# Kernel tuning notes

Hardware: AMD Instinct MI355X
Metric: run time of the kernel (lower is better)

The kernel has to match this reference:

```python
import jax, jax.numpy as jnp
import numpy as np

B, T, C = 2, 2048, 2048
E, K, S, F = 8, 2, 1, 1408
AUX_COEF, Z_COEF = 0.01, 0.001


def setup_inputs() -> dict:
    key = jax.random.key(0)
    ks = jax.random.split(key, 8)
    sc = 1.0 / np.sqrt(C)
    sf = 1.0 / np.sqrt(F)
    return {
        "x": jax.random.normal(ks[0], (B, T, C), jnp.float32),
        "gate_w": jax.random.normal(ks[1], (E, C), jnp.float32) * sc,   # torch Linear weight [out,in]
        "w1": jax.random.normal(ks[2], (E, F, C), jnp.float32) * sc,    # routed expert up-proj
        "w2": jax.random.normal(ks[3], (E, C, F), jnp.float32) * sf,    # routed expert down-proj
        "sw1": jax.random.normal(ks[4], (S, F, C), jnp.float32) * sc,   # shared expert up-proj
        "sw2": jax.random.normal(ks[5], (S, C, F), jnp.float32) * sf,   # shared expert down-proj
        "alpha": jnp.ones((C,), jnp.float32),                            # HyperConnection scale on MoE out
        "beta": jnp.ones((C,), jnp.float32),                             # HyperConnection scale on residual x
    }


def reference(x, gate_w, w1, w2, sw1, sw2, alpha, beta):
    Bv, Tv, Cv = x.shape
    xf = x.reshape(-1, Cv)                                  # [N, C]
    logits = xf @ gate_w.T                                  # [N, E]
    probs = jax.nn.softmax(logits, axis=-1)
    weights, selected = jax.lax.top_k(probs, K)             # [N, K]
    weights = weights / jnp.sum(weights, axis=-1, keepdims=True)
    aux_loss = AUX_COEF * jnp.sum(jnp.mean(probs, axis=0) ** 2)
    z_loss = Z_COEF * jnp.mean(jax.nn.logsumexp(logits, axis=-1) ** 2)
    # combine[n, e] = routing weight of expert e for token n (0 if not selected)
    combine = jnp.sum(jax.nn.one_hot(selected, E, dtype=xf.dtype) * weights[..., None], axis=1)  # [N, E]
    out = jnp.zeros_like(xf)
    for e in range(E):  # fixed small expert count; weight is 0 for unrouted tokens
        h = jax.nn.silu(xf @ w1[e].T) @ w2[e].T             # [N, C]
        out = out + combine[:, e:e + 1] * h
    for s in range(S):
        out = out + jax.nn.silu(xf @ sw1[s].T) @ sw2[s].T
    y = alpha * out.reshape(Bv, Tv, Cv) + beta * x           # HyperConnection residual mix
    return y, aux_loss + z_loss
```

## Files before the change

kernel.cpp:

```cpp
#include <hip/hip_runtime.h>


#define TOKS 4096
#define CD 2048
#define FD 1408
#define RROWS 8192
#define NTMAX 104

typedef unsigned short u16;
typedef float f32x4 __attribute__((ext_vector_type(4)));
typedef __bf16 bf16x8 __attribute__((ext_vector_type(8)));

__device__ __forceinline__ u16 f2bf(float f) {
  unsigned u = __float_as_uint(f);
  u += 0x7fffu + ((u >> 16) & 1u);
  return (u16)(u >> 16);
}

__global__ __launch_bounds__(256) void gate_kernel(
    const float* __restrict__ x, const float* __restrict__ gw,
    float* __restrict__ combine, float* __restrict__ part, int* __restrict__ sel,
    u16* __restrict__ xb)
{
  const int lane = threadIdx.x & 63;
  const int wave = threadIdx.x >> 6;
  const int n = blockIdx.x * 4 + wave;
  const float* xr = x + (size_t)n * CD;
  u16* xbr = xb + (size_t)n * CD;
  float p[8] = {0,0,0,0,0,0,0,0};
#pragma unroll
  for (int it = 0; it < 8; ++it) {
    const int idx = it * 256 + lane * 4;
    const float4 xv = *(const float4*)(xr + idx);
    ushort4 xo;
    xo.x = f2bf(xv.x); xo.y = f2bf(xv.y); xo.z = f2bf(xv.z); xo.w = f2bf(xv.w);
    *(ushort4*)(xbr + idx) = xo;
#pragma unroll
    for (int e = 0; e < 8; ++e) {
      const float4 gv = *(const float4*)(gw + e * CD + idx);
      p[e] += xv.x * gv.x + xv.y * gv.y + xv.z * gv.z + xv.w * gv.w;
    }
  }
#pragma unroll
  for (int e = 0; e < 8; ++e) {
#pragma unroll
    for (int m = 32; m > 0; m >>= 1) p[e] += __shfl_xor(p[e], m, 64);
  }
  float mx = p[0];
#pragma unroll
  for (int e = 1; e < 8; ++e) mx = fmaxf(mx, p[e]);
  float s = 0.f, pr[8];
#pragma unroll
  for (int e = 0; e < 8; ++e) { pr[e] = __expf(p[e] - mx); s += pr[e]; }
  const float inv = 1.f / s;
#pragma unroll
  for (int e = 0; e < 8; ++e) pr[e] *= inv;
  const float lse = mx + __logf(s);
  int i1 = 0;
#pragma unroll
  for (int e = 1; e < 8; ++e) if (pr[e] > pr[i1]) i1 = e;
  int i2 = (i1 == 0) ? 1 : 0;
#pragma unroll
  for (int e = 0; e < 8; ++e) if (e != i1 && pr[e] > pr[i2]) i2 = e;
  const float rs = 1.f / (pr[i1] + pr[i2]);

  __shared__ float pl[4][12];
  if (lane == 0) {
    float* cr = combine + (size_t)n * 16;
#pragma unroll
    for (int e = 0; e < 8; ++e) cr[e] = 0.f;
    cr[i1] = pr[i1] * rs;
    cr[i2] = pr[i2] * rs;
    cr[8] = 1.0f;
    sel[n] = i1 | (i2 << 4);
#pragma unroll
    for (int e = 0; e < 8; ++e) pl[wave][e] = pr[e];
    pl[wave][8] = lse * lse;
  }
  __syncthreads();
  if (threadIdx.x < 9)
    part[(size_t)blockIdx.x * 16 + threadIdx.x] =
        pl[0][threadIdx.x] + pl[1][threadIdx.x] + pl[2][threadIdx.x] + pl[3][threadIdx.x];
}

__global__ void route_kernel(const int* __restrict__ sel, int* __restrict__ le,
                             int* __restrict__ pos, int* __restrict__ cntoff,
                             int* __restrict__ tileMap)
{
  const int lane = threadIdx.x;
  const unsigned long long lt = (1ull << lane) - 1ull;
  int cnt[8] = {0,0,0,0,0,0,0,0};
  for (int c = 0; c < TOKS / 64; ++c) {
    const int s = sel[c * 64 + lane];
    const int e1 = s & 15, e2 = (s >> 4) & 15;
#pragma unroll
    for (int e = 0; e < 8; ++e)
      cnt[e] += __popcll(__ballot(e1 == e)) + __popcll(__ballot(e2 == e));
  }
  int off[8]; off[0] = 0;
#pragma unroll
  for (int e = 1; e < 8; ++e) off[e] = off[e - 1] + cnt[e - 1];
  int base[8];
#pragma unroll
  for (int e = 0; e < 8; ++e) base[e] = off[e];
  for (int c = 0; c < TOKS / 64; ++c) {
    const int n = c * 64 + lane;
    const int s = sel[n];
    const int e1 = s & 15, e2 = (s >> 4) & 15;
#pragma unroll
    for (int e = 0; e < 8; ++e) {
      const unsigned long long m1 = __ballot(e1 == e);
      const unsigned long long m2 = __ballot(e2 == e);
      if (e1 == e) { const int r = base[e] + __popcll(m1 & lt); le[r] = n; pos[2 * n] = r; }
      if (e2 == e) { const int r = base[e] + __popcll(m1) + __popcll(m2 & lt); le[r] = n; pos[2 * n + 1] = r; }
      base[e] += __popcll(m1) + __popcll(m2);
    }
  }
  if (lane < 8) { cntoff[lane] = cnt[lane]; cntoff[16 + lane] = off[lane]; }
  if (lane == 8) { cntoff[8] = TOKS; cntoff[24] = RROWS; }
  if (lane == 0) {
    int t = 0;
    for (int e = 0; e < 8; ++e)
      for (int m = 0; m < cnt[e]; m += 128) tileMap[t++] = e | (m << 4);
    for (int m = 0; m < TOKS; m += 128) tileMap[t++] = 8 | (m << 4);
    cntoff[25] = t;
  }
}

__global__ void finalize_kernel(const float* __restrict__ part, float* __restrict__ loss_out)
{
  __shared__ float sm[256][10];
  float loc[9] = {0,0,0,0,0,0,0,0,0};
  for (int b = threadIdx.x; b < 1024; b += 256)
#pragma unroll
    for (int c = 0; c < 9; ++c) loc[c] += part[(size_t)b * 16 + c];
#pragma unroll
  for (int c = 0; c < 9; ++c) sm[threadIdx.x][c] = loc[c];
  __syncthreads();
  for (int off = 128; off > 0; off >>= 1) {
    if (threadIdx.x < off)
#pragma unroll
      for (int c = 0; c < 9; ++c) sm[threadIdx.x][c] += sm[threadIdx.x + off][c];
    __syncthreads();
  }
  if (threadIdx.x == 0) {
    float aux = 0.f;
#pragma unroll
    for (int e = 0; e < 8; ++e) { const float m = sm[0][e] * (1.f / TOKS); aux += m * m; }
    const float z = sm[0][8] * (1.f / TOKS);
    loss_out[0] = 0.01f * aux + 0.001f * z;
  }
}

#define W14  5767168
#define SW14 720896
__global__ void cast_all_kernel(const float4* __restrict__ w1, const float4* __restrict__ sw1,
                                const float4* __restrict__ w2, const float4* __restrict__ sw2,
                                u16* __restrict__ w1b, u16* __restrict__ w2b)
{
  const int total = 2 * (W14 + SW14);
  int i = blockIdx.x * blockDim.x + threadIdx.x;
  const int stride = gridDim.x * blockDim.x;
  for (; i < total; i += stride) {
    int j = i;
    const float4* src; u16* dst;
    if (j < W14)                   { src = w1;  dst = w1b; }
    else if ((j -= W14) < SW14)    { src = sw1; dst = w1b + (size_t)8 * FD * CD; }
    else if ((j -= SW14) < W14)    { src = w2;  dst = w2b; }
    else                           { j -= W14; src = sw2; dst = w2b + (size_t)8 * CD * FD; }
    const float4 v = src[j];
    ushort4 o;
    o.x = f2bf(v.x); o.y = f2bf(v.y); o.z = f2bf(v.z); o.w = f2bf(v.w);
    *(ushort4*)(dst + (size_t)j * 4) = o;
  }
}

template<int MODE, int MINW>
__global__ __launch_bounds__(256, MINW) void gemm_bt(
    const u16* __restrict__ Abase, const u16* __restrict__ Bbase,
    u16* __restrict__ outBF, const float* __restrict__ combine,
    const int* __restrict__ le, const int* __restrict__ cntoff,
    const int* __restrict__ tileMap)
{
  constexpr int K  = (MODE == 0) ? CD : FD;
  constexpr int OS = (MODE == 0) ? FD : CD;
  constexpr int NY = (MODE == 0) ? 11 : 16;
  constexpr int Q  = NTMAX * NY / 8;

  __shared__ __attribute__((aligned(16))) u16 smA[128 * 64];
  __shared__ __attribute__((aligned(16))) u16 smB[128 * 64];

  const int orig = blockIdx.x + gridDim.x * blockIdx.y;
  const int wgid = (orig & 7) * Q + (orig >> 3);
  const int t = wgid / NY;
  const int y = wgid - t * NY;
  const int NT = cntoff[25];
  if (t >= NT) return;
  const int packed = tileMap[t];
  const int e = packed & 15;
  const int m0 = packed >> 4;
  const int cnt = cntoff[e];
  const int off = cntoff[16 + e];
  const int n0 = y * 128;

  const int tid = threadIdx.x;
  const int lane = tid & 63;
  const int wave = tid >> 6;
  const int wr = wave >> 1, wc = wave & 1;

  const u16* A = (MODE == 0) ? Abase : (Abase + (size_t)off * FD);
  const u16* Bp = Bbase + (size_t)e * FD * CD;

  const int sub_r = lane >> 3;
  const int sub_c = (lane & 7) << 3;

  int arow[4];
#pragma unroll
  for (int r = 0; r < 4; ++r) {
    const int lr = (wave * 4 + r) * 8 + sub_r;
    if (MODE == 0)
      arow[r] = (e == 8) ? (m0 + lr) : ((m0 + lr < cnt) ? le[off + m0 + lr] : 0);
    else
      arow[r] = m0 + lr;
  }

  f32x4 acc[4][4] = {};

  const int nkt = K >> 6;
  for (int kt = 0; kt < nkt; ++kt) {
    const int k0 = kt << 6;
#pragma unroll
    for (int r = 0; r < 4; ++r) {
      const int ch = (wave << 2) + r;
      const u16* ga = A + (size_t)arow[r] * K + k0 + sub_c;
      const u16* gb = Bp + (size_t)(n0 + ch * 8 + sub_r) * K + k0 + sub_c;
      __builtin_amdgcn_global_load_lds((const __attribute__((address_space(1))) void*)ga,
                                       (__attribute__((address_space(3))) void*)(smA + ch * 512),
                                       16, 0, 0);
      __builtin_amdgcn_global_load_lds((const __attribute__((address_space(1))) void*)gb,
                                       (__attribute__((address_space(3))) void*)(smB + ch * 512),
                                       16, 0, 0);
    }
    asm volatile("s_waitcnt vmcnt(0)" ::: "memory");
    __syncthreads();
#pragma unroll
    for (int kk = 0; kk < 2; ++kk) {
      const int ko = (kk << 5) + ((lane >> 4) << 3);
      bf16x8 af[4];
#pragma unroll
      for (int i = 0; i < 4; ++i)
        af[i] = *(const bf16x8*)(smA + ((wr * 64 + i * 16 + (lane & 15)) << 6) + ko);
#pragma unroll
      for (int j = 0; j < 4; ++j) {
        const bf16x8 bv = *(const bf16x8*)(smB + ((wc * 64 + j * 16 + (lane & 15)) << 6) + ko);
#pragma unroll
        for (int i = 0; i < 4; ++i)
          acc[i][j] = __builtin_amdgcn_mfma_f32_16x16x32_bf16(af[i], bv, acc[i][j], 0, 0, 0);
      }
    }
    __syncthreads();
  }

#pragma unroll
  for (int i = 0; i < 4; ++i) {
    const int rloc0 = wr * 64 + i * 16 + ((lane >> 4) << 2);
#pragma unroll
    for (int q = 0; q < 4; ++q) {
      const int rloc = rloc0 + q;
      if (m0 + rloc >= cnt) continue;
      float sc = 1.f;
      if (MODE == 0) {
        const int tok = (e == 8) ? (m0 + rloc) : le[off + m0 + rloc];
        sc = combine[(size_t)tok * 16 + e];
      }
#pragma unroll
      for (int j = 0; j < 4; ++j) {
        const int col = n0 + wc * 64 + j * 16 + (lane & 15);
        const float v = acc[i][j][q];
        const float h = (MODE == 0) ? (sc * v * (1.f / (1.f + __expf(-v)))) : v;
        outBF[(size_t)(off + m0 + rloc) * OS + col] = f2bf(h);
      }
    }
  }
}

__global__ __launch_bounds__(256) void gather_kernel(
    const u16* __restrict__ Yc, const int* __restrict__ pos,
    const float* __restrict__ x, const float* __restrict__ alpha,
    const float* __restrict__ beta, float* __restrict__ out)
{
  const int n = blockIdx.x;
  const int c0 = threadIdx.x * 8;
  const int p1 = pos[2 * n], p2 = pos[2 * n + 1];
  const bf16x8 a = *(const bf16x8*)(Yc + (size_t)p1 * CD + c0);
  const bf16x8 b = *(const bf16x8*)(Yc + (size_t)p2 * CD + c0);
  const bf16x8 s = *(const bf16x8*)(Yc + ((size_t)RROWS + n) * CD + c0);
  const float* xr = x + (size_t)n * CD + c0;
  float* orow = out + (size_t)n * CD + c0;
#pragma unroll
  for (int j = 0; j < 8; ++j) {
    const float v = (float)a[j] + (float)b[j] + (float)s[j];
    orow[j] = alpha[c0 + j] * v + beta[c0 + j] * xr[j];
  }
}

extern "C" void kernel_launch(void* const* d_in, const int* in_sizes, int n_in,
                              void* d_out, int out_size, void* d_ws, size_t ws_size,
                              hipStream_t stream)
{
  (void)in_sizes; (void)n_in; (void)out_size; (void)ws_size;
  const float* x     = (const float*)d_in[0];
  const float* gw    = (const float*)d_in[1];
  const float* w1    = (const float*)d_in[2];
  const float* w2    = (const float*)d_in[3];
  const float* sw1   = (const float*)d_in[4];
  const float* sw2   = (const float*)d_in[5];
  const float* alpha = (const float*)d_in[6];
  const float* beta  = (const float*)d_in[7];
  float* out = (float*)d_out;

  char* ws = (char*)d_ws;
  float* combine = (float*)(ws + 0);
  float* part    = (float*)(ws + 262144);
  int*   sel     = (int*)(ws + 327680);
  int*   le      = (int*)(ws + 344064);
  int*   pos     = (int*)(ws + 376832);
  int*   cntoff  = (int*)(ws + 409600);
  int*   tileMap = (int*)(ws + 409856);
  u16*   xb      = (u16*)(ws + 410368);
  u16*   w1b     = (u16*)(ws + 17187584);
  u16*   w2b     = (u16*)(ws + 69092096);
  u16*   Hcomp   = (u16*)(ws + 120996608);
  u16*   Ycomp   = (u16*)(ws + 155599616);

  gate_kernel<<<1024, 256, 0, stream>>>(x, gw, combine, part, sel, xb);
  route_kernel<<<1, 64, 0, stream>>>(sel, le, pos, cntoff, tileMap);
  finalize_kernel<<<1, 256, 0, stream>>>(part, out + (size_t)TOKS * CD);
  cast_all_kernel<<<4096, 256, 0, stream>>>((const float4*)w1, (const float4*)sw1,
                                            (const float4*)w2, (const float4*)sw2, w1b, w2b);
  gemm_bt<0, 5><<<dim3(NTMAX, 11), 256, 0, stream>>>(xb, w1b, Hcomp, combine, le, cntoff, tileMap);
  gemm_bt<1, 4><<<dim3(NTMAX, 16), 256, 0, stream>>>(Hcomp, w2b, Ycomp, nullptr, nullptr, cntoff, tileMap);
  gather_kernel<<<TOKS, 256, 0, stream>>>(Ycomp, pos, x, alpha, beta, out);
}
```

Before: 498.3 us.

## Triple-buffer grouped GEMM with 256-row tiles, XOR-swizzled LDS and 512 threads

Reworks the grouped expert GEMM so each workgroup covers 256 token rows with 512 threads (8 waves). It uses a three-stage LDS ring filled by global_load_lds, with partial vmcnt waits so loads run two K-steps ahead of the MFMA work. LDS columns are XOR-swizzled to cut bank conflicts, and MFMA sections get raised priority. The aim is to hide global memory latency and halve B-operand traffic per row. The cost is more LDS use, fewer workgroups, more padding waste on small expert tiles, and out-of-range A rows that are clamped rather than skipped.

```diff
diff --git a/kernel.cpp b/kernel.cpp
--- a/kernel.cpp
+++ b/kernel.cpp
@@ -5,7 +5,7 @@
 #define CD 2048
 #define FD 1408
 #define RROWS 8192
-#define NTMAX 104
+#define NT256 56
 
 typedef unsigned short u16;
 typedef float f32x4 __attribute__((ext_vector_type(4)));
@@ -121,8 +121,8 @@
   if (lane == 0) {
     int t = 0;
     for (int e = 0; e < 8; ++e)
-      for (int m = 0; m < cnt[e]; m += 128) tileMap[t++] = e | (m << 4);
-    for (int m = 0; m < TOKS; m += 128) tileMap[t++] = 8 | (m << 4);
+      for (int m = 0; m < cnt[e]; m += 256) tileMap[t++] = e | (m << 4);
+    for (int m = 0; m < TOKS; m += 256) tileMap[t++] = 8 | (m << 4);
     cntoff[25] = t;
   }
 }
@@ -175,20 +175,21 @@
   }
 }
 
-template<int MODE, int MINW>
-__global__ __launch_bounds__(256, MINW) void gemm_bt(
+template<int MODE>
+__global__ __launch_bounds__(512, 2) void gemm_bt(
     const u16* __restrict__ Abase, const u16* __restrict__ Bbase,
     u16* __restrict__ outBF, const float* __restrict__ combine,
     const int* __restrict__ le, const int* __restrict__ cntoff,
     const int* __restrict__ tileMap)
 {
-  constexpr int K  = (MODE == 0) ? CD : FD;
-  constexpr int OS = (MODE == 0) ? FD : CD;
-  constexpr int NY = (MODE == 0) ? 11 : 16;
-  constexpr int Q  = NTMAX * NY / 8;
-
-  __shared__ __attribute__((aligned(16))) u16 smA[128 * 64];
-  __shared__ __attribute__((aligned(16))) u16 smB[128 * 64];
+  constexpr int K   = (MODE == 0) ? CD : FD;
+  constexpr int OS  = (MODE == 0) ? FD : CD;
+  constexpr int NY  = (MODE == 0) ? 11 : 16;
+  constexpr int NKT = K >> 6;
+  constexpr int Q   = NT256 * NY / 8;
+
+  __shared__ __attribute__((aligned(16))) u16 smA[3][256 * 64];
+  __shared__ __attribute__((aligned(16))) u16 smB[3][128 * 64];
 
   const int orig = blockIdx.x + gridDim.x * blockIdx.y;
   const int wgid = (orig & 7) * Q + (orig >> 3);
@@ -203,67 +204,106 @@
   const int off = cntoff[16 + e];
   const int n0 = y * 128;
 
-  const int tid = threadIdx.x;
+  const int tid  = threadIdx.x;
   const int lane = tid & 63;
   const int wave = tid >> 6;
-  const int wr = wave >> 1, wc = wave & 1;
-
-  const u16* A = (MODE == 0) ? Abase : (Abase + (size_t)off * FD);
+  const int wm = wave >> 1;
+  const int wn = wave & 1;
+
   const u16* Bp = Bbase + (size_t)e * FD * CD;
 
-  const int sub_r = lane >> 3;
-  const int sub_c = (lane & 7) << 3;
-
-  int arow[4];
-#pragma unroll
-  for (int r = 0; r < 4; ++r) {
-    const int lr = (wave * 4 + r) * 8 + sub_r;
+  const int srow = wave * 8 + (lane >> 3);
+  const int gcol = (((lane & 7) ^ ((lane >> 3) & 7)) << 3);
+
+  const u16* pAg[4];
+#pragma unroll
+  for (int c = 0; c < 4; ++c) {
+    const int r = m0 + c * 64 + srow;
+    long arow;
     if (MODE == 0)
-      arow[r] = (e == 8) ? (m0 + lr) : ((m0 + lr < cnt) ? le[off + m0 + lr] : 0);
+      arow = (e == 8) ? r : le[min(off + r, RROWS - 1)];
     else
-      arow[r] = m0 + lr;
-  }
+      arow = min(off + r, RROWS + TOKS - 1);
+    pAg[c] = Abase + (size_t)arow * K + gcol;
+  }
+  const u16* pBg[2];
+#pragma unroll
+  for (int c = 0; c < 2; ++c)
+    pBg[c] = Bp + (size_t)(n0 + c * 64 + srow) * K + gcol;
+
+  auto STG = [&](u16* pa, u16* pb, int kt) {
+    const int kof = kt << 6;
+#pragma unroll
+    for (int c = 0; c < 4; ++c)
+      __builtin_amdgcn_global_load_lds(
+          (const __attribute__((address_space(1))) void*)(pAg[c] + kof),
+          (__attribute__((address_space(3))) void*)(pa + c * 4096 + wave * 512), 16, 0, 0);
+#pragma unroll
+    for (int c = 0; c < 2; ++c)
+      __builtin_amdgcn_global_load_lds(
+          (const __attribute__((address_space(1))) void*)(pBg[c] + kof),
+          (__attribute__((address_space(3))) void*)(pb + c * 4096 + wave * 512), 16, 0, 0);
+  };
+
+  u16 *pa0 = smA[0], *pa1 = smA[1], *pa2 = smA[2];
+  u16 *pb0 = smB[0], *pb1 = smB[1], *pb2 = smB[2];
 
   f32x4 acc[4][4] = {};
 
-  const int nkt = K >> 6;
-  for (int kt = 0; kt < nkt; ++kt) {
-    const int k0 = kt << 6;
-#pragma unroll
-    for (int r = 0; r < 4; ++r) {
-      const int ch = (wave << 2) + r;
-      const u16* ga = A + (size_t)arow[r] * K + k0 + sub_c;
-      const u16* gb = Bp + (size_t)(n0 + ch * 8 + sub_r) * K + k0 + sub_c;
-      __builtin_amdgcn_global_load_lds((const __attribute__((address_space(1))) void*)ga,
-                                       (__attribute__((address_space(3))) void*)(smA + ch * 512),
-                                       16, 0, 0);
-      __builtin_amdgcn_global_load_lds((const __attribute__((address_space(1))) void*)gb,
-                                       (__attribute__((address_space(3))) void*)(smB + ch * 512),
-                                       16, 0, 0);
-    }
-    asm volatile("s_waitcnt vmcnt(0)" ::: "memory");
-    __syncthreads();
+  STG(pa0, pb0, 0);
+  STG(pa1, pb1, 1);
+
+  const int la15 = lane & 15;
+  const int g16  = lane >> 4;
+
+#pragma unroll 1
+  for (int kt = 0; kt < NKT; ++kt) {
+    if (kt + 2 < NKT) {
+      STG(pa2, pb2, kt + 2);
+      asm volatile("s_waitcnt vmcnt(12)" ::: "memory");
+    } else if (kt + 2 == NKT) {
+      asm volatile("s_waitcnt vmcnt(6)" ::: "memory");
+    } else {
+      asm volatile("s_waitcnt vmcnt(0)" ::: "memory");
+    }
+    asm volatile("" ::: "memory");
+    __builtin_amdgcn_s_barrier();
+    asm volatile("" ::: "memory");
+
 #pragma unroll
     for (int kk = 0; kk < 2; ++kk) {
-      const int ko = (kk << 5) + ((lane >> 4) << 3);
-      bf16x8 af[4];
+      const int gg = (kk << 2) + g16;
+      bf16x8 af[4], bv[4];
+#pragma unroll
+      for (int i = 0; i < 4; ++i) {
+        const int r = wm * 64 + i * 16 + la15;
+        af[i] = *(const bf16x8*)(pa0 + r * 64 + ((gg ^ (r & 7)) << 3));
+      }
+#pragma unroll
+      for (int j = 0; j < 4; ++j) {
+        const int r = wn * 64 + j * 16 + la15;
+        bv[j] = *(const bf16x8*)(pb0 + r * 64 + ((gg ^ (r & 7)) << 3));
+      }
+      __builtin_amdgcn_s_setprio(1);
 #pragma unroll
       for (int i = 0; i < 4; ++i)
-        af[i] = *(const bf16x8*)(smA + ((wr * 64 + i * 16 + (lane & 15)) << 6) + ko);
-#pragma unroll
-      for (int j = 0; j < 4; ++j) {
-        const bf16x8 bv = *(const bf16x8*)(smB + ((wc * 64 + j * 16 + (lane & 15)) << 6) + ko);
-#pragma unroll
-        for (int i = 0; i < 4; ++i)
-          acc[i][j] = __builtin_amdgcn_mfma_f32_16x16x32_bf16(af[i], bv, acc[i][j], 0, 0, 0);
-      }
-    }
-    __syncthreads();
+#pragma unroll
+        for (int j = 0; j < 4; ++j)
+          acc[i][j] = __builtin_amdgcn_mfma_f32_16x16x32_bf16(af[i], bv[j], acc[i][j], 0, 0, 0);
+      __builtin_amdgcn_s_setprio(0);
+    }
+
+    asm volatile("" ::: "memory");
+    __builtin_amdgcn_s_barrier();
+    asm volatile("" ::: "memory");
+
+    u16* ta = pa0; pa0 = pa1; pa1 = pa2; pa2 = ta;
+    u16* tb = pb0; pb0 = pb1; pb1 = pb2; pb2 = tb;
   }
 
 #pragma unroll
   for (int i = 0; i < 4; ++i) {
-    const int rloc0 = wr * 64 + i * 16 + ((lane >> 4) << 2);
+    const int rloc0 = wm * 64 + i * 16 + (g16 << 2);
 #pragma unroll
     for (int q = 0; q < 4; ++q) {
       const int rloc = rloc0 + q;
@@ -275,7 +315,7 @@
       }
 #pragma unroll
       for (int j = 0; j < 4; ++j) {
-        const int col = n0 + wc * 64 + j * 16 + (lane & 15);
+        const int col = n0 + wn * 64 + j * 16 + la15;
         const float v = acc[i][j][q];
         const float h = (MODE == 0) ? (sc * v * (1.f / (1.f + __expf(-v)))) : v;
         outBF[(size_t)(off + m0 + rloc) * OS + col] = f2bf(h);
@@ -338,7 +378,7 @@
   finalize_kernel<<<1, 256, 0, stream>>>(part, out + (size_t)TOKS * CD);
   cast_all_kernel<<<4096, 256, 0, stream>>>((const float4*)w1, (const float4*)sw1,
                                             (const float4*)w2, (const float4*)sw2, w1b, w2b);
-  gemm_bt<0, 5><<<dim3(NTMAX, 11), 256, 0, stream>>>(xb, w1b, Hcomp, combine, le, cntoff, tileMap);
-  gemm_bt<1, 4><<<dim3(NTMAX, 16), 256, 0, stream>>>(Hcomp, w2b, Ycomp, nullptr, nullptr, cntoff, tileMap);
+  gemm_bt<0><<<dim3(NT256, 11), 512, 0, stream>>>(xb, w1b, Hcomp, combine, le, cntoff, tileMap);
+  gemm_bt<1><<<dim3(NT256, 16), 512, 0, stream>>>(Hcomp, w2b, Ycomp, nullptr, nullptr, cntoff, tileMap);
   gather_kernel<<<TOKS, 256, 0, stream>>>(Ycomp, pos, x, alpha, beta, out);
 }
```

New measurement: 458.6 us. -8.0%, faster.

## Switch expert GEMMs to 256x256 tiles with double-buffered swizzled LDS and 8 waves

Applied to the files above, without the earlier changes.

Replaces the 128x128 single-buffered expert GEMM with a 512-thread kernel that computes 256x256 tiles. It double-buffers LDS with staged prefetch interleaved across four compute phases, XOR-swizzles the LDS layout to avoid bank conflicts, and raises MFMA priority with setprio. The up-projection weights are padded to 1536 rows so the N dimension divides into 256-wide tiles, with padded columns skipped at store time. The larger tiles improve data reuse and overlap loads with compute, but they add padding waste, partially empty M tiles for smaller experts, and fewer workgroups.

```diff
diff --git a/kernel.cpp b/kernel.cpp
--- a/kernel.cpp
+++ b/kernel.cpp
@@ -4,8 +4,9 @@
 #define TOKS 4096
 #define CD 2048
 #define FD 1408
+#define FDP 1536
 #define RROWS 8192
-#define NTMAX 104
+#define NT256 56
 
 typedef unsigned short u16;
 typedef float f32x4 __attribute__((ext_vector_type(4)));
@@ -121,8 +122,8 @@
   if (lane == 0) {
     int t = 0;
     for (int e = 0; e < 8; ++e)
-      for (int m = 0; m < cnt[e]; m += 128) tileMap[t++] = e | (m << 4);
-    for (int m = 0; m < TOKS; m += 128) tileMap[t++] = 8 | (m << 4);
+      for (int m = 0; m < cnt[e]; m += 256) tileMap[t++] = e | (m << 4);
+    for (int m = 0; m < TOKS; m += 256) tileMap[t++] = 8 | (m << 4);
     cntoff[25] = t;
   }
 }
@@ -152,121 +153,172 @@
   }
 }
 
-#define W14  5767168
-#define SW14 720896
-__global__ void cast_all_kernel(const float4* __restrict__ w1, const float4* __restrict__ sw1,
-                                const float4* __restrict__ w2, const float4* __restrict__ sw2,
+#define S1E  786432
+#define S2E  720896
+__global__ void cast_all_kernel(const float* __restrict__ w1, const float* __restrict__ sw1,
+                                const float* __restrict__ w2, const float* __restrict__ sw2,
                                 u16* __restrict__ w1b, u16* __restrict__ w2b)
 {
-  const int total = 2 * (W14 + SW14);
+  const int total = 9 * (S1E + S2E);
   int i = blockIdx.x * blockDim.x + threadIdx.x;
   const int stride = gridDim.x * blockDim.x;
   for (; i < total; i += stride) {
-    int j = i;
-    const float4* src; u16* dst;
-    if (j < W14)                   { src = w1;  dst = w1b; }
-    else if ((j -= W14) < SW14)    { src = sw1; dst = w1b + (size_t)8 * FD * CD; }
-    else if ((j -= SW14) < W14)    { src = w2;  dst = w2b; }
-    else                           { j -= W14; src = sw2; dst = w2b + (size_t)8 * CD * FD; }
-    const float4 v = src[j];
     ushort4 o;
-    o.x = f2bf(v.x); o.y = f2bf(v.y); o.z = f2bf(v.z); o.w = f2bf(v.w);
-    *(ushort4*)(dst + (size_t)j * 4) = o;
-  }
-}
-
-template<int MODE, int MINW>
-__global__ __launch_bounds__(256, MINW) void gemm_bt(
+    u16* dst;
+    if (i < 9 * S1E) {
+      const int e = i / S1E, rem = i - e * S1E;
+      const int r = rem >> 9, g = rem & 511;
+      dst = w1b + ((size_t)e * FDP + r) * CD + g * 4;
+      if (r < FD) {
+        const float* src = (e < 8) ? (w1 + ((size_t)e * FD + r) * CD) : (sw1 + (size_t)r * CD);
+        const float4 v = *(const float4*)(src + g * 4);
+        o.x = f2bf(v.x); o.y = f2bf(v.y); o.z = f2bf(v.z); o.w = f2bf(v.w);
+      } else {
+        o.x = o.y = o.z = o.w = 0;
+      }
+    } else {
+      const int j = i - 9 * S1E;
+      const int e = j / S2E, rem = j - e * S2E;
+      const int r = rem / 352, g = rem % 352;
+      const float* src = (e < 8) ? (w2 + ((size_t)e * CD + r) * FD) : (sw2 + (size_t)r * FD);
+      const float4 v = *(const float4*)(src + g * 4);
+      o.x = f2bf(v.x); o.y = f2bf(v.y); o.z = f2bf(v.z); o.w = f2bf(v.w);
+      dst = w2b + ((size_t)e * CD + r) * FD + g * 4;
+    }
+    *(ushort4*)dst = o;
+  }
+}
+
+
+#define LDSR(base, r, gg) (*(const bf16x8*)((base) + (r) * 64 + ((((gg) ^ ((r) & 7))) << 3)))
+
+#define PHASE(mh, nh, STG)                                                                     \
+  {                                                                                            \
+    asm volatile("" ::: "memory");                                                             \
+    __builtin_amdgcn_s_barrier();                                                              \
+    asm volatile("" ::: "memory");                                                             \
+    STG;                                                                                       \
+    const u16* sa_ = &smA[cur][0];                                                             \
+    const u16* sb_ = &smB[cur][0];                                                             \
+    _Pragma("unroll")                                                                          \
+    for (int kk = 0; kk < 2; ++kk) {                                                           \
+      const int gg = kk * 4 + g16;                                                             \
+      const int ra = (mh) * 128 + wm * 64 + la15;                                              \
+      const int rb = (nh) * 128 + wn * 32 + la15;                                              \
+      const bf16x8 af0 = LDSR(sa_, ra,      gg);                                               \
+      const bf16x8 af1 = LDSR(sa_, ra + 16, gg);                                               \
+      const bf16x8 af2 = LDSR(sa_, ra + 32, gg);                                               \
+      const bf16x8 af3 = LDSR(sa_, ra + 48, gg);                                               \
+      const bf16x8 bv0 = LDSR(sb_, rb,      gg);                                               \
+      const bf16x8 bv1 = LDSR(sb_, rb + 16, gg);                                               \
+      __builtin_amdgcn_s_setprio(1);                                                           \
+      acc[(mh)*4+0][(nh)*2+0] = __builtin_amdgcn_mfma_f32_16x16x32_bf16(af0, bv0, acc[(mh)*4+0][(nh)*2+0], 0, 0, 0); \
+      acc[(mh)*4+1][(nh)*2+0] = __builtin_amdgcn_mfma_f32_16x16x32_bf16(af1, bv0, acc[(mh)*4+1][(nh)*2+0], 0, 0, 0); \
+      acc[(mh)*4+2][(nh)*2+0] = __builtin_amdgcn_mfma_f32_16x16x32_bf16(af2, bv0, acc[(mh)*4+2][(nh)*2+0], 0, 0, 0); \
+      acc[(mh)*4+3][(nh)*2+0] = __builtin_amdgcn_mfma_f32_16x16x32_bf16(af3, bv0, acc[(mh)*4+3][(nh)*2+0], 0, 0, 0); \
+      acc[(mh)*4+0][(nh)*2+1] = __builtin_amdgcn_mfma_f32_16x16x32_bf16(af0, bv1, acc[(mh)*4+0][(nh)*2+1], 0, 0, 0); \
+      acc[(mh)*4+1][(nh)*2+1] = __builtin_amdgcn_mfma_f32_16x16x32_bf16(af1, bv1, acc[(mh)*4+1][(nh)*2+1], 0, 0, 0); \
+      acc[(mh)*4+2][(nh)*2+1] = __builtin_amdgcn_mfma_f32_16x16x32_bf16(af2, bv1, acc[(mh)*4+2][(nh)*2+1], 0, 0, 0); \
+      acc[(mh)*4+3][(nh)*2+1] = __builtin_amdgcn_mfma_f32_16x16x32_bf16(af3, bv1, acc[(mh)*4+3][(nh)*2+1], 0, 0, 0); \
+      __builtin_amdgcn_s_setprio(0);                                                           \
+    }                                                                                          \
+  }
+
+template<int MODE>
+__global__ __launch_bounds__(512, 2) void gemm8p(
     const u16* __restrict__ Abase, const u16* __restrict__ Bbase,
     u16* __restrict__ outBF, const float* __restrict__ combine,
     const int* __restrict__ le, const int* __restrict__ cntoff,
     const int* __restrict__ tileMap)
 {
-  constexpr int K  = (MODE == 0) ? CD : FD;
-  constexpr int OS = (MODE == 0) ? FD : CD;
-  constexpr int NY = (MODE == 0) ? 11 : 16;
-  constexpr int Q  = NTMAX * NY / 8;
-
-  __shared__ __attribute__((aligned(16))) u16 smA[128 * 64];
-  __shared__ __attribute__((aligned(16))) u16 smB[128 * 64];
+  constexpr int K   = (MODE == 0) ? CD : FD;
+  constexpr int BS  = (MODE == 0) ? FDP : CD;
+  constexpr int OS  = (MODE == 0) ? FD : CD;
+  constexpr int NY  = (MODE == 0) ? 6 : 8;
+  constexpr int NKT = K >> 6;
+  constexpr int Q   = NT256 * NY / 8;
+
+  __shared__ __attribute__((aligned(16))) u16 smA[2][256 * 64];
+  __shared__ __attribute__((aligned(16))) u16 smB[2][256 * 64];
 
   const int orig = blockIdx.x + gridDim.x * blockIdx.y;
   const int wgid = (orig & 7) * Q + (orig >> 3);
-  const int t = wgid / NY;
-  const int y = wgid - t * NY;
+  const int tix = wgid / NY;
+  const int y = wgid - tix * NY;
   const int NT = cntoff[25];
-  if (t >= NT) return;
-  const int packed = tileMap[t];
+  if (tix >= NT) return;
+  const int packed = tileMap[tix];
   const int e = packed & 15;
   const int m0 = packed >> 4;
   const int cnt = cntoff[e];
   const int off = cntoff[16 + e];
-  const int n0 = y * 128;
-
-  const int tid = threadIdx.x;
-  const int lane = tid & 63;
-  const int wave = tid >> 6;
-  const int wr = wave >> 1, wc = wave & 1;
-
-  const u16* A = (MODE == 0) ? Abase : (Abase + (size_t)off * FD);
-  const u16* Bp = Bbase + (size_t)e * FD * CD;
-
-  const int sub_r = lane >> 3;
-  const int sub_c = (lane & 7) << 3;
-
-  int arow[4];
-#pragma unroll
-  for (int r = 0; r < 4; ++r) {
-    const int lr = (wave * 4 + r) * 8 + sub_r;
-    if (MODE == 0)
-      arow[r] = (e == 8) ? (m0 + lr) : ((m0 + lr < cnt) ? le[off + m0 + lr] : 0);
-    else
-      arow[r] = m0 + lr;
-  }
-
-  f32x4 acc[4][4] = {};
-
-  const int nkt = K >> 6;
-  for (int kt = 0; kt < nkt; ++kt) {
-    const int k0 = kt << 6;
-#pragma unroll
-    for (int r = 0; r < 4; ++r) {
-      const int ch = (wave << 2) + r;
-      const u16* ga = A + (size_t)arow[r] * K + k0 + sub_c;
-      const u16* gb = Bp + (size_t)(n0 + ch * 8 + sub_r) * K + k0 + sub_c;
-      __builtin_amdgcn_global_load_lds((const __attribute__((address_space(1))) void*)ga,
-                                       (__attribute__((address_space(3))) void*)(smA + ch * 512),
-                                       16, 0, 0);
-      __builtin_amdgcn_global_load_lds((const __attribute__((address_space(1))) void*)gb,
-                                       (__attribute__((address_space(3))) void*)(smB + ch * 512),
-                                       16, 0, 0);
-    }
-    asm volatile("s_waitcnt vmcnt(0)" ::: "memory");
-    __syncthreads();
-#pragma unroll
-    for (int kk = 0; kk < 2; ++kk) {
-      const int ko = (kk << 5) + ((lane >> 4) << 3);
-      bf16x8 af[4];
-#pragma unroll
-      for (int i = 0; i < 4; ++i)
-        af[i] = *(const bf16x8*)(smA + ((wr * 64 + i * 16 + (lane & 15)) << 6) + ko);
-#pragma unroll
-      for (int j = 0; j < 4; ++j) {
-        const bf16x8 bv = *(const bf16x8*)(smB + ((wc * 64 + j * 16 + (lane & 15)) << 6) + ko);
-#pragma unroll
-        for (int i = 0; i < 4; ++i)
-          acc[i][j] = __builtin_amdgcn_mfma_f32_16x16x32_bf16(af[i], bv, acc[i][j], 0, 0, 0);
-      }
-    }
-    __syncthreads();
-  }
-
-#pragma unroll
-  for (int i = 0; i < 4; ++i) {
-    const int rloc0 = wr * 64 + i * 16 + ((lane >> 4) << 2);
+  const int n0 = y * 256;
+
+  const int tid  = threadIdx.x;
+  const int ln   = tid & 63;
+  const int wv   = tid >> 6;
+  const int wm   = wv >> 2;
+  const int wn   = wv & 3;
+  const int la15 = ln & 15;
+  const int g16  = ln >> 4;
+
+  const u16* Bp = Bbase + (size_t)e * (size_t)BS * K;
+
+  const int srow = ln >> 3;
+  const int sgrp = (((ln & 7) ^ srow) << 3);
+  const u16* pA[2][2];
+  const u16* pB[2][2];
+#pragma unroll
+  for (int h = 0; h < 2; ++h)
+#pragma unroll
+    for (int l = 0; l < 2; ++l) {
+      const int rloc = h * 128 + (wv * 2 + l) * 8 + srow;
+      size_t arow;
+      if (MODE == 0)
+        arow = (e == 8) ? (size_t)(m0 + rloc)
+                        : (size_t)le[min(off + m0 + rloc, RROWS - 1)];
+      else
+        arow = (size_t)(off + m0 + rloc);
+      pA[h][l] = Abase + arow * K + sgrp;
+      pB[h][l] = Bp + (size_t)(n0 + h * 128 + (wv * 2 + l) * 8 + srow) * K + sgrp;
+    }
+
+#define SA(buf, h, kt)                                                                         \
+  _Pragma("unroll")                                                                            \
+  for (int l_ = 0; l_ < 2; ++l_)                                                               \
+    __builtin_amdgcn_global_load_lds(                                                          \
+        (const __attribute__((address_space(1))) void*)(pA[h][l_] + (kt) * 64),                \
+        (__attribute__((address_space(3))) void*)(&smA[buf][(h) * 8192 + (wv * 2 + l_) * 512]),\
+        16, 0, 0);
+#define SB(buf, h, kt)                                                                         \
+  _Pragma("unroll")                                                                            \
+  for (int l_ = 0; l_ < 2; ++l_)                                                               \
+    __builtin_amdgcn_global_load_lds(                                                          \
+        (const __attribute__((address_space(1))) void*)(pB[h][l_] + (kt) * 64),                \
+        (__attribute__((address_space(3))) void*)(&smB[buf][(h) * 8192 + (wv * 2 + l_) * 512]),\
+        16, 0, 0);
+
+  f32x4 acc[8][4] = {};
+
+  SA(0, 0, 0); SB(0, 1, 0); SA(0, 1, 0); SB(0, 0, 0); SA(1, 0, 1); SB(1, 1, 1);
+
+#pragma unroll 1
+  for (int t = 0; t < NKT; ++t) {
+    const int cur = t & 1;
+    if (t < NKT - 1) { asm volatile("s_waitcnt vmcnt(4)" ::: "memory"); }
+    else             { asm volatile("s_waitcnt vmcnt(0)" ::: "memory"); }
+    PHASE(0, 0, if (t + 1 < NKT) { SA(cur ^ 1, 1, t + 1) })
+    PHASE(0, 1, if (t + 1 < NKT) { SB(cur ^ 1, 0, t + 1) })
+    PHASE(1, 1, if (t + 2 < NKT) { SA(cur, 0, t + 2) })
+    PHASE(1, 0, if (t + 2 < NKT) { SB(cur, 1, t + 2) })
+  }
+
+#pragma unroll
+  for (int mi = 0; mi < 8; ++mi) {
+    const int rq = (mi >> 2) * 128 + wm * 64 + (mi & 3) * 16 + g16 * 4;
 #pragma unroll
     for (int q = 0; q < 4; ++q) {
-      const int rloc = rloc0 + q;
+      const int rloc = rq + q;
       if (m0 + rloc >= cnt) continue;
       float sc = 1.f;
       if (MODE == 0) {
@@ -274,14 +326,17 @@
         sc = combine[(size_t)tok * 16 + e];
       }
 #pragma unroll
-      for (int j = 0; j < 4; ++j) {
-        const int col = n0 + wc * 64 + j * 16 + (lane & 15);
-        const float v = acc[i][j][q];
+      for (int ni = 0; ni < 4; ++ni) {
+        const int col = n0 + (ni >> 1) * 128 + wn * 32 + (ni & 1) * 16 + la15;
+        if (MODE == 0 && col >= FD) continue;
+        const float v = acc[mi][ni][q];
         const float h = (MODE == 0) ? (sc * v * (1.f / (1.f + __expf(-v)))) : v;
         outBF[(size_t)(off + m0 + rloc) * OS + col] = f2bf(h);
       }
     }
   }
+#undef SA
+#undef SB
 }
 
 __global__ __launch_bounds__(256) void gather_kernel(
@@ -329,16 +384,15 @@
   int*   tileMap = (int*)(ws + 409856);
   u16*   xb      = (u16*)(ws + 410368);
   u16*   w1b     = (u16*)(ws + 17187584);
-  u16*   w2b     = (u16*)(ws + 69092096);
-  u16*   Hcomp   = (u16*)(ws + 120996608);
-  u16*   Ycomp   = (u16*)(ws + 155599616);
+  u16*   w2b     = (u16*)(ws + 73810688);
+  u16*   Hcomp   = (u16*)(ws + 125715200);
+  u16*   Ycomp   = (u16*)(ws + 160318208);
 
   gate_kernel<<<1024, 256, 0, stream>>>(x, gw, combine, part, sel, xb);
   route_kernel<<<1, 64, 0, stream>>>(sel, le, pos, cntoff, tileMap);
   finalize_kernel<<<1, 256, 0, stream>>>(part, out + (size_t)TOKS * CD);
-  cast_all_kernel<<<4096, 256, 0, stream>>>((const float4*)w1, (const float4*)sw1,
-                                            (const float4*)w2, (const float4*)sw2, w1b, w2b);
-  gemm_bt<0, 5><<<dim3(NTMAX, 11), 256, 0, stream>>>(xb, w1b, Hcomp, combine, le, cntoff, tileMap);
-  gemm_bt<1, 4><<<dim3(NTMAX, 16), 256, 0, stream>>>(Hcomp, w2b, Ycomp, nullptr, nullptr, cntoff, tileMap);
+  cast_all_kernel<<<4096, 256, 0, stream>>>(w1, sw1, w2, sw2, w1b, w2b);
+  gemm8p<0><<<dim3(NT256, 6), 512, 0, stream>>>(xb, w1b, Hcomp, combine, le, cntoff, tileMap);
+  gemm8p<1><<<dim3(NT256, 8), 512, 0, stream>>>(Hcomp, w2b, Ycomp, nullptr, nullptr, cntoff, tileMap);
   gather_kernel<<<TOKS, 256, 0, stream>>>(Ycomp, pos, x, alpha, beta, out);
 }
```

Result: slower. 524.2 us (+5.2%).

## Double-buffer LDS tiles with XOR swizzle in expert GEMMs

Applied to the files above, without the earlier changes.

The expert GEMM kernel now keeps two LDS buffers per operand and prefetches the next K-tile while running MFMAs on the current one, leaving one barrier per iteration instead of two. LDS column groups are XOR-swizzled by row to cut bank conflicts on the fragment reads. Launch bounds drop to 2 waves per SIMD because LDS use doubles to 64KB, which lowers occupancy in exchange for overlapping loads with compute. Gathered row indices are clamped instead of zeroed for padded rows.

```diff
diff --git a/kernel.cpp b/kernel.cpp
--- a/kernel.cpp
+++ b/kernel.cpp
@@ -175,20 +175,21 @@
   }
 }
 
-template<int MODE, int MINW>
-__global__ __launch_bounds__(256, MINW) void gemm_bt(
+template<int MODE>
+__global__ __launch_bounds__(256, 2) void gemm_bt(
     const u16* __restrict__ Abase, const u16* __restrict__ Bbase,
     u16* __restrict__ outBF, const float* __restrict__ combine,
     const int* __restrict__ le, const int* __restrict__ cntoff,
     const int* __restrict__ tileMap)
 {
-  constexpr int K  = (MODE == 0) ? CD : FD;
-  constexpr int OS = (MODE == 0) ? FD : CD;
-  constexpr int NY = (MODE == 0) ? 11 : 16;
-  constexpr int Q  = NTMAX * NY / 8;
-
-  __shared__ __attribute__((aligned(16))) u16 smA[128 * 64];
-  __shared__ __attribute__((aligned(16))) u16 smB[128 * 64];
+  constexpr int K   = (MODE == 0) ? CD : FD;
+  constexpr int OS  = (MODE == 0) ? FD : CD;
+  constexpr int NY  = (MODE == 0) ? 11 : 16;
+  constexpr int NKT = K >> 6;
+  constexpr int Q   = NTMAX * NY / 8;
+
+  __shared__ __attribute__((aligned(16))) u16 smA[2][128 * 64];
+  __shared__ __attribute__((aligned(16))) u16 smB[2][128 * 64];
 
   const int orig = blockIdx.x + gridDim.x * blockIdx.y;
   const int wgid = (orig & 7) * Q + (orig >> 3);
@@ -203,67 +204,93 @@
   const int off = cntoff[16 + e];
   const int n0 = y * 128;
 
-  const int tid = threadIdx.x;
-  const int lane = tid & 63;
-  const int wave = tid >> 6;
-  const int wr = wave >> 1, wc = wave & 1;
-
-  const u16* A = (MODE == 0) ? Abase : (Abase + (size_t)off * FD);
+  const int tid  = threadIdx.x;
+  const int ln   = tid & 63;
+  const int wv   = tid >> 6;
+  const int wr   = wv >> 1, wc = wv & 1;
+  const int la15 = ln & 15;
+  const int g16  = ln >> 4;
+
   const u16* Bp = Bbase + (size_t)e * FD * CD;
 
-  const int sub_r = lane >> 3;
-  const int sub_c = (lane & 7) << 3;
-
-  int arow[4];
-#pragma unroll
-  for (int r = 0; r < 4; ++r) {
-    const int lr = (wave * 4 + r) * 8 + sub_r;
+  const int srow = ln >> 3;
+  const int sgrp = (((ln & 7) ^ srow) << 3);
+  const u16* pA[4];
+  const u16* pB[4];
+#pragma unroll
+  for (int c = 0; c < 4; ++c) {
+    const int rloc = c * 32 + wv * 8 + srow;
+    size_t arow;
     if (MODE == 0)
-      arow[r] = (e == 8) ? (m0 + lr) : ((m0 + lr < cnt) ? le[off + m0 + lr] : 0);
+      arow = (e == 8) ? (size_t)(m0 + rloc)
+                      : (size_t)le[min(off + m0 + rloc, RROWS - 1)];
     else
-      arow[r] = m0 + lr;
+      arow = (size_t)(off + m0 + rloc);
+    pA[c] = Abase + arow * K + sgrp;
+    pB[c] = Bp + (size_t)(n0 + rloc) * K + sgrp;
+  }
+
+#define STAGE(buf, kt)                                                                        \
+  {                                                                                           \
+    const int kof_ = (kt) << 6;                                                               \
+    _Pragma("unroll")                                                                         \
+    for (int c_ = 0; c_ < 4; ++c_) {                                                          \
+      __builtin_amdgcn_global_load_lds(                                                       \
+          (const __attribute__((address_space(1))) void*)(pA[c_] + kof_),                     \
+          (__attribute__((address_space(3))) void*)(&smA[buf][c_ * 2048 + wv * 512]),         \
+          16, 0, 0);                                                                          \
+      __builtin_amdgcn_global_load_lds(                                                       \
+          (const __attribute__((address_space(1))) void*)(pB[c_] + kof_),                     \
+          (__attribute__((address_space(3))) void*)(&smB[buf][c_ * 2048 + wv * 512]),         \
+          16, 0, 0);                                                                          \
+    }                                                                                         \
   }
 
   f32x4 acc[4][4] = {};
 
-  const int nkt = K >> 6;
-  for (int kt = 0; kt < nkt; ++kt) {
-    const int k0 = kt << 6;
-#pragma unroll
-    for (int r = 0; r < 4; ++r) {
-      const int ch = (wave << 2) + r;
-      const u16* ga = A + (size_t)arow[r] * K + k0 + sub_c;
-      const u16* gb = Bp + (size_t)(n0 + ch * 8 + sub_r) * K + k0 + sub_c;
-      __builtin_amdgcn_global_load_lds((const __attribute__((address_space(1))) void*)ga,
-                                       (__attribute__((address_space(3))) void*)(smA + ch * 512),
-                                       16, 0, 0);
-      __builtin_amdgcn_global_load_lds((const __attribute__((address_space(1))) void*)gb,
-                                       (__attribute__((address_space(3))) void*)(smB + ch * 512),
-                                       16, 0, 0);
-    }
-    asm volatile("s_waitcnt vmcnt(0)" ::: "memory");
-    __syncthreads();
+  STAGE(0, 0)
+  asm volatile("s_waitcnt vmcnt(0)" ::: "memory");
+  __builtin_amdgcn_s_barrier();
+  asm volatile("" ::: "memory");
+
+#pragma unroll 1
+  for (int kt = 0; kt < NKT; ++kt) {
+    const int cur = kt & 1;
+    if (kt + 1 < NKT) STAGE(cur ^ 1, kt + 1)
+    const u16* sa = &smA[cur][0];
+    const u16* sb = &smB[cur][0];
 #pragma unroll
     for (int kk = 0; kk < 2; ++kk) {
-      const int ko = (kk << 5) + ((lane >> 4) << 3);
-      bf16x8 af[4];
+      const int gg = kk * 4 + g16;
+      bf16x8 af[4], bv[4];
+#pragma unroll
+      for (int i = 0; i < 4; ++i) {
+        const int r = wr * 64 + i * 16 + la15;
+        af[i] = *(const bf16x8*)(sa + r * 64 + (((gg ^ (r & 7))) << 3));
+      }
+#pragma unroll
+      for (int j = 0; j < 4; ++j) {
+        const int r = wc * 64 + j * 16 + la15;
+        bv[j] = *(const bf16x8*)(sb + r * 64 + (((gg ^ (r & 7))) << 3));
+      }
 #pragma unroll
       for (int i = 0; i < 4; ++i)
-        af[i] = *(const bf16x8*)(smA + ((wr * 64 + i * 16 + (lane & 15)) << 6) + ko);
-#pragma unroll
-      for (int j = 0; j < 4; ++j) {
-        const bf16x8 bv = *(const bf16x8*)(smB + ((wc * 64 + j * 16 + (lane & 15)) << 6) + ko);
-#pragma unroll
-        for (int i = 0; i < 4; ++i)
-          acc[i][j] = __builtin_amdgcn_mfma_f32_16x16x32_bf16(af[i], bv, acc[i][j], 0, 0, 0);
-      }
-    }
-    __syncthreads();
-  }
+#pragma unroll
+        for (int j = 0; j < 4; ++j)
+          acc[i][j] = __builtin_amdgcn_mfma_f32_16x16x32_bf16(af[i], bv[j], acc[i][j], 0, 0, 0);
+    }
+    if (kt + 1 < NKT) {
+      asm volatile("s_waitcnt vmcnt(0)" ::: "memory");
+      asm volatile("" ::: "memory");
+      __builtin_amdgcn_s_barrier();
+      asm volatile("" ::: "memory");
+    }
+  }
+#undef STAGE
 
 #pragma unroll
   for (int i = 0; i < 4; ++i) {
-    const int rloc0 = wr * 64 + i * 16 + ((lane >> 4) << 2);
+    const int rloc0 = wr * 64 + i * 16 + (g16 << 2);
 #pragma unroll
     for (int q = 0; q < 4; ++q) {
       const int rloc = rloc0 + q;
@@ -275,7 +302,7 @@
       }
 #pragma unroll
       for (int j = 0; j < 4; ++j) {
-        const int col = n0 + wc * 64 + j * 16 + (lane & 15);
+        const int col = n0 + wc * 64 + j * 16 + la15;
         const float v = acc[i][j][q];
         const float h = (MODE == 0) ? (sc * v * (1.f / (1.f + __expf(-v)))) : v;
         outBF[(size_t)(off + m0 + rloc) * OS + col] = f2bf(h);
@@ -338,7 +365,7 @@
   finalize_kernel<<<1, 256, 0, stream>>>(part, out + (size_t)TOKS * CD);
   cast_all_kernel<<<4096, 256, 0, stream>>>((const float4*)w1, (const float4*)sw1,
                                             (const float4*)w2, (const float4*)sw2, w1b, w2b);
-  gemm_bt<0, 5><<<dim3(NTMAX, 11), 256, 0, stream>>>(xb, w1b, Hcomp, combine, le, cntoff, tileMap);
-  gemm_bt<1, 4><<<dim3(NTMAX, 16), 256, 0, stream>>>(Hcomp, w2b, Ycomp, nullptr, nullptr, cntoff, tileMap);
+  gemm_bt<0><<<dim3(NTMAX, 11), 256, 0, stream>>>(xb, w1b, Hcomp, combine, le, cntoff, tileMap);
+  gemm_bt<1><<<dim3(NTMAX, 16), 256, 0, stream>>>(Hcomp, w2b, Ycomp, nullptr, nullptr, cntoff, tileMap);
   gather_kernel<<<TOKS, 256, 0, stream>>>(Ycomp, pos, x, alpha, beta, out);
 }
```

Result: faster. 410.6 us (-17.6%).
